# Optimization experiments

Hardware: AMD Instinct MI355X
Metric: run time of the kernel (lower is better)

## Reference

```python
import jax, jax.numpy as jnp
import numpy as np

NEG_SLOPE = 0.2

def setup_inputs() -> dict:
    key = jax.random.key(0)
    k1, k2, k3, k4, k5 = jax.random.split(key, 5)
    N_src, N_dst, E, H, D = 50000, 50000, 1600000, 8, 16
    return {
        "h_src": jax.random.normal(k1, (N_src, H * D), dtype=jnp.float32),
        "h_dst": jax.random.normal(k2, (N_dst, H * D), dtype=jnp.float32),
        "attn_l": jax.random.normal(k3, (1, H, D), dtype=jnp.float32),
        "src": jax.random.randint(k4, (E,), 0, N_src, dtype=jnp.int32),
        "dst": jax.random.randint(k5, (E,), 0, N_dst, dtype=jnp.int32),
    }

def reference(h_src, h_dst, attn_l, src, dst):
    N_dst = h_dst.shape[0]
    H, D = attn_l.shape[1], attn_l.shape[2]
    hs = h_src.reshape(-1, H, D)                       # [N_src, H, D]
    el = jnp.sum(hs * attn_l, axis=-1)                 # [N_src, H] per-node attn logit
    e = jax.nn.leaky_relu(el[src], NEG_SLOPE)          # [E, H] per-edge score
    # edge softmax over incoming edges of each dst node (stable)
    seg_max = jax.ops.segment_max(e, dst, num_segments=N_dst)   # [N_dst, H]
    ex = jnp.exp(e - seg_max[dst])                     # [E, H]
    denom = jax.ops.segment_sum(ex, dst, num_segments=N_dst)    # [N_dst, H]
    a = ex / denom[dst]                                # [E, H]
    # gather-multiply-scatter: u_mul_e then sum by dst
    m = hs[src] * a[:, :, None]                        # [E, H, D]
    out = jax.ops.segment_sum(m, dst, num_segments=N_dst)       # [N_dst, H, D]
    return out.reshape(N_dst, H * D)
```

## Files before the change

### kernel.cpp

```cpp
#include <hip/hip_runtime.h>

#define Hh 8
#define HD 128
#define NEG_SLOPE 0.2f
#define EPB 4096
#define GRS 197


__device__ __forceinline__ unsigned bfr(float f) {
    unsigned u = __float_as_uint(f);
    return (u + 0x7fffu + ((u >> 16) & 1u)) >> 16;
}
__device__ __forceinline__ unsigned pk(float a, float b) { return bfr(a) | (bfr(b) << 16); }

__global__ void __launch_bounds__(1024)
k1(const int* __restrict__ src, const int* __restrict__ dst,
   unsigned* __restrict__ tmp, unsigned short* __restrict__ ghs,
   int* __restrict__ bktTot, int E, int nblk,
   const float* __restrict__ hs, const float* __restrict__ attn,
   float* __restrict__ ew, uint4* __restrict__ hsb, int nh_src) {
    int t = threadIdx.x;
    if ((int)blockIdx.x < nblk) {
        __shared__ unsigned wbuf[EPB];
        __shared__ int lh[256], cur[256];
        int blk = blockIdx.x;
        int base = blk * EPB;
        int cnt = E - base; if (cnt > EPB) cnt = EPB;
        if (t < 256) lh[t] = 0;
        __syncthreads();
        int i = t * 4;
        bool vec = (i + 3 < cnt);
        if (vec) {
            int4 d = *(const int4*)(dst + base + i);
            int4 s = *(const int4*)(src + base + i);
            uint4 w;
            w.x = ((unsigned)d.x << 16) | (unsigned)s.x;
            w.y = ((unsigned)d.y << 16) | (unsigned)s.y;
            w.z = ((unsigned)d.z << 16) | (unsigned)s.z;
            w.w = ((unsigned)d.w << 16) | (unsigned)s.w;
            ((uint4*)wbuf)[t] = w;
            atomicAdd(&lh[d.x >> 8], 1);
            atomicAdd(&lh[d.y >> 8], 1);
            atomicAdd(&lh[d.z >> 8], 1);
            atomicAdd(&lh[d.w >> 8], 1);
        } else {
            for (int e = i; e < cnt; ++e) {
                int d = dst[base + e];
                wbuf[e] = ((unsigned)d << 16) | (unsigned)src[base + e];
                atomicAdd(&lh[d >> 8], 1);
            }
        }
        __syncthreads();
        int v = 0;
        if (t < 256) { v = lh[t]; cur[t] = v; }
        __syncthreads();
        for (int off = 1; off < 256; off <<= 1) {
            int x = 0;
            if (t < 256 && t >= off) x = cur[t - off];
            __syncthreads();
            if (t < 256) cur[t] += x;
            __syncthreads();
        }
        if (t < GRS) ghs[(size_t)blk * GRS + t] = (unsigned short)(cur[t] - ((t < 256) ? v : 0));
        if (t < 196 && v) atomicAdd(&bktTot[t], v);
        if (t < 256) cur[t] -= v;
        __syncthreads();
        if (vec) {
            uint4 w = ((uint4*)wbuf)[t];
            int p;
            p = atomicAdd(&cur[w.x >> 24], 1); tmp[base + p] = w.x;
            p = atomicAdd(&cur[w.y >> 24], 1); tmp[base + p] = w.y;
            p = atomicAdd(&cur[w.z >> 24], 1); tmp[base + p] = w.z;
            p = atomicAdd(&cur[w.w >> 24], 1); tmp[base + p] = w.w;
        } else {
            for (int e = i; e < cnt; ++e) {
                unsigned w = wbuf[e];
                int p = atomicAdd(&cur[w >> 24], 1);
                tmp[base + p] = w;
            }
        }
    } else {
        int i = ((int)blockIdx.x - nblk) * 1024 + t;
        if (i >= nh_src) return;
        int n = i >> 3, h = i & 7;
        const float4* a = (const float4*)(hs + (size_t)n * HD + h * 16);
        const float4* w = (const float4*)(attn + h * 16);
        float4 x0 = a[0], x1 = a[1], x2 = a[2], x3 = a[3];
        float4 w0 = w[0], w1 = w[1], w2 = w[2], w3 = w[3];
        float sv = x0.x * w0.x + x0.y * w0.y + x0.z * w0.z + x0.w * w0.w
                 + x1.x * w1.x + x1.y * w1.y + x1.z * w1.z + x1.w * w1.w
                 + x2.x * w2.x + x2.y * w2.y + x2.z * w2.z + x2.w * w2.w
                 + x3.x * w3.x + x3.y * w3.y + x3.z * w3.z + x3.w * w3.w;
        sv = (sv >= 0.f) ? sv : NEG_SLOPE * sv;
        ew[i] = __expf(sv);
        uint4 p0 = { pk(x0.x, x0.y), pk(x0.z, x0.w), pk(x1.x, x1.y), pk(x1.z, x1.w) };
        uint4 p1 = { pk(x2.x, x2.y), pk(x2.z, x2.w), pk(x3.x, x3.y), pk(x3.z, x3.w) };
        hsb[(size_t)n * 16 + h * 2]     = p0;
        hsb[(size_t)n * 16 + h * 2 + 1] = p1;
    }
}

__global__ void __launch_bounds__(1024)
k2(const unsigned* __restrict__ tmp, const unsigned short* __restrict__ ghs,
   const int* __restrict__ bktTot, unsigned short* __restrict__ adj,
   int* __restrict__ row_ptr, int E, int nblk, int nbkt, int ndst) {
    __shared__ int lh[256], sh[256], cur[256];
    __shared__ int base_s;
    int b = blockIdx.x, t = threadIdx.x;
    if (t < 256) lh[t] = 0;
    __syncthreads();
    for (int blk = t; blk < nblk; blk += 1024) {
        const unsigned short* gr = ghs + (size_t)blk * GRS;
        int st = gr[b], en = gr[b + 1];
        const unsigned* tp = tmp + (size_t)blk * EPB;
        for (int j = st; j < en; ++j)
            atomicAdd(&lh[(tp[j] >> 16) & 255], 1);
    }
    __syncthreads();
    int bc = 0;
    if (t < 256) { bc = (t < nbkt) ? bktTot[t] : 0; sh[t] = bc; }
    __syncthreads();
    for (int off = 1; off < 256; off <<= 1) {
        int x = 0;
        if (t < 256 && t >= off) x = sh[t - off];
        __syncthreads();
        if (t < 256) sh[t] += x;
        __syncthreads();
    }
    if (t == b) base_s = sh[t] - bc;
    __syncthreads();
    int base_b = base_s;
    int v = 0;
    if (t < 256) { v = lh[t]; sh[t] = v; }
    __syncthreads();
    for (int off = 1; off < 256; off <<= 1) {
        int x = 0;
        if (t < 256 && t >= off) x = sh[t - off];
        __syncthreads();
        if (t < 256) sh[t] += x;
        __syncthreads();
    }
    if (t < 256) {
        int start = base_b + sh[t] - v;
        cur[t] = start;
        int d = b * 256 + t;
        if (d < ndst) row_ptr[d] = start;
        if (b == 0 && t == 0) row_ptr[ndst] = E;
    }
    __syncthreads();
    for (int blk = t; blk < nblk; blk += 1024) {
        const unsigned short* gr = ghs + (size_t)blk * GRS;
        int st = gr[b], en = gr[b + 1];
        const unsigned* tp = tmp + (size_t)blk * EPB;
        for (int j = st; j < en; ++j) {
            unsigned w = tp[j];
            int pos = atomicAdd(&cur[(w >> 16) & 255], 1);
            adj[pos] = (unsigned short)(w & 0xffff);
        }
    }
}

#define ACC8(X, W) \
    a0.x += __uint_as_float((X).x << 16) * (W); \
    a0.y += __uint_as_float((X).x & 0xffff0000u) * (W); \
    a0.z += __uint_as_float((X).y << 16) * (W); \
    a0.w += __uint_as_float((X).y & 0xffff0000u) * (W); \
    a1.x += __uint_as_float((X).z << 16) * (W); \
    a1.y += __uint_as_float((X).z & 0xffff0000u) * (W); \
    a1.z += __uint_as_float((X).w << 16) * (W); \
    a1.w += __uint_as_float((X).w & 0xffff0000u) * (W);

__global__ void __launch_bounds__(128)
k_agg(const int* __restrict__ row_ptr, const unsigned short* __restrict__ adj,
      const uint4* __restrict__ hsb, const float* __restrict__ ew,
      float* __restrict__ out) {
    int d = blockIdx.x;
    int t = threadIdx.x;
    int j0 = row_ptr[d], j1 = row_ptr[d + 1];
    int q = t & 15;
    int slot = t >> 4;
    int h = q >> 1;

    float4 a0 = {0.f, 0.f, 0.f, 0.f}, a1 = {0.f, 0.f, 0.f, 0.f};
    float ws = 0.f;
    int j = j0 + slot;
    for (; j + 24 < j1; j += 32) {
        int s0 = adj[j], s1 = adj[j + 8], s2 = adj[j + 16], s3 = adj[j + 24];
        float w0 = ew[s0 * Hh + h], w1 = ew[s1 * Hh + h];
        float w2 = ew[s2 * Hh + h], w3 = ew[s3 * Hh + h];
        uint4 x0 = hsb[(size_t)s0 * 16 + q];
        uint4 x1 = hsb[(size_t)s1 * 16 + q];
        uint4 x2 = hsb[(size_t)s2 * 16 + q];
        uint4 x3 = hsb[(size_t)s3 * 16 + q];
        ACC8(x0, w0)
        ACC8(x1, w1)
        ACC8(x2, w2)
        ACC8(x3, w3)
        ws += w0 + w1 + w2 + w3;
    }
    for (; j < j1; j += 8) {
        int s0 = adj[j];
        float w0 = ew[s0 * Hh + h];
        uint4 x0 = hsb[(size_t)s0 * 16 + q];
        ACC8(x0, w0)
        ws += w0;
    }

#pragma unroll
    for (int off = 16; off <= 32; off <<= 1) {
        a0.x += __shfl_xor(a0.x, off, 64);
        a0.y += __shfl_xor(a0.y, off, 64);
        a0.z += __shfl_xor(a0.z, off, 64);
        a0.w += __shfl_xor(a0.w, off, 64);
        a1.x += __shfl_xor(a1.x, off, 64);
        a1.y += __shfl_xor(a1.y, off, 64);
        a1.z += __shfl_xor(a1.z, off, 64);
        a1.w += __shfl_xor(a1.w, off, 64);
        ws   += __shfl_xor(ws,   off, 64);
    }
    __shared__ float4 sp0[16], sp1[16];
    __shared__ float wsp[16];
    if (t >= 64 && t < 80) { sp0[q] = a0; sp1[q] = a1; wsp[q] = ws; }
    __syncthreads();
    if (t < 16) {
        float wt = ws + wsp[t];
        float r = (wt > 0.f) ? 1.0f / wt : 0.f;
        float4 o0 = sp0[t], o1 = sp1[t];
        o0.x = (a0.x + o0.x) * r; o0.y = (a0.y + o0.y) * r;
        o0.z = (a0.z + o0.z) * r; o0.w = (a0.w + o0.w) * r;
        o1.x = (a1.x + o1.x) * r; o1.y = (a1.y + o1.y) * r;
        o1.z = (a1.z + o1.z) * r; o1.w = (a1.w + o1.w) * r;
        float4* op = (float4*)(out + (size_t)d * HD + t * 8);
        op[0] = o0;
        op[1] = o1;
    }
}

extern "C" void kernel_launch(void* const* d_in, const int* in_sizes, int n_in,
                              void* d_out, int out_size, void* d_ws, size_t ws_size,
                              hipStream_t stream) {
    const float* h_src  = (const float*)d_in[0];
    const float* attn_l = (const float*)d_in[2];
    const int*   src    = (const int*)d_in[3];
    const int*   dst    = (const int*)d_in[4];
    float* out = (float*)d_out;

    const int N_src = in_sizes[0] / HD;
    const int N_dst = in_sizes[1] / HD;
    const int E     = in_sizes[3];
    const int NH_src = N_src * Hh;

    const int NBLK  = (E + EPB - 1) / EPB;
    const int NBKT  = (N_dst + 255) / 256;
    const int NB_EW = (NH_src + 1023) / 1024;

    unsigned short* hsb = (unsigned short*)d_ws;
    float* ew = (float*)(hsb + (size_t)N_src * HD);
    unsigned* tmp = (unsigned*)(ew + NH_src);
    unsigned short* adj = (unsigned short*)(tmp + (size_t)NBLK * EPB);
    unsigned short* ghs = adj + (((size_t)E + 1) & ~(size_t)1);
    int* bktTot  = (int*)(ghs + (((size_t)NBLK * GRS + 1) & ~(size_t)1));
    int* row_ptr = bktTot + 256;

    hipMemsetAsync(bktTot, 0, 256 * sizeof(int), stream);
    k1<<<NBLK + NB_EW, 1024, 0, stream>>>(src, dst, tmp, ghs, bktTot, E, NBLK,
                                          h_src, attn_l, ew, (uint4*)hsb, NH_src);
    k2<<<NBKT, 1024, 0, stream>>>(tmp, ghs, bktTot, adj, row_ptr,
                                  E, NBLK, NBKT, N_dst);
    k_agg<<<N_dst, 128, 0, stream>>>(row_ptr, adj, (const uint4*)hsb, ew, out);
}
```

Baseline: 213.1 us.

## Bin edges into fixed-capacity dst buckets and fuse local sort with aggregation

```diff
diff --git a/kernel.cpp b/kernel.cpp
--- a/kernel.cpp
+++ b/kernel.cpp
@@ -4,7 +4,7 @@
 #define HD 128
 #define NEG_SLOPE 0.2f
 #define EPB 4096
-#define GRS 197
+#define KCAP 2560
 
 
 __device__ __forceinline__ unsigned bfr(float f) {
@@ -15,18 +15,17 @@
 
 __global__ void __launch_bounds__(1024)
 k1(const int* __restrict__ src, const int* __restrict__ dst,
-   unsigned* __restrict__ tmp, unsigned short* __restrict__ ghs,
-   int* __restrict__ bktTot, int E, int nblk,
+   unsigned* __restrict__ tmp, int* __restrict__ blen,
+   int E, int nblk, int nbf,
    const float* __restrict__ hs, const float* __restrict__ attn,
    float* __restrict__ ew, uint4* __restrict__ hsb, int nh_src) {
     int t = threadIdx.x;
     if ((int)blockIdx.x < nblk) {
         __shared__ unsigned wbuf[EPB];
-        __shared__ int lh[256], cur[256];
-        int blk = blockIdx.x;
-        int base = blk * EPB;
+        __shared__ int lh[800], cur[800];
+        int base = blockIdx.x * EPB;
         int cnt = E - base; if (cnt > EPB) cnt = EPB;
-        if (t < 256) lh[t] = 0;
+        if (t < 800) lh[t] = 0;
         __syncthreads();
         int i = t * 4;
         bool vec = (i + 3 < cnt);
@@ -39,44 +38,36 @@
             w.z = ((unsigned)d.z << 16) | (unsigned)s.z;
             w.w = ((unsigned)d.w << 16) | (unsigned)s.w;
             ((uint4*)wbuf)[t] = w;
-            atomicAdd(&lh[d.x >> 8], 1);
-            atomicAdd(&lh[d.y >> 8], 1);
-            atomicAdd(&lh[d.z >> 8], 1);
-            atomicAdd(&lh[d.w >> 8], 1);
+            atomicAdd(&lh[d.x >> 6], 1);
+            atomicAdd(&lh[d.y >> 6], 1);
+            atomicAdd(&lh[d.z >> 6], 1);
+            atomicAdd(&lh[d.w >> 6], 1);
         } else {
             for (int e = i; e < cnt; ++e) {
                 int d = dst[base + e];
                 wbuf[e] = ((unsigned)d << 16) | (unsigned)src[base + e];
-                atomicAdd(&lh[d >> 8], 1);
+                atomicAdd(&lh[d >> 6], 1);
             }
         }
         __syncthreads();
-        int v = 0;
-        if (t < 256) { v = lh[t]; cur[t] = v; }
-        __syncthreads();
-        for (int off = 1; off < 256; off <<= 1) {
-            int x = 0;
-            if (t < 256 && t >= off) x = cur[t - off];
-            __syncthreads();
-            if (t < 256) cur[t] += x;
-            __syncthreads();
-        }
-        if (t < GRS) ghs[(size_t)blk * GRS + t] = (unsigned short)(cur[t] - ((t < 256) ? v : 0));
-        if (t < 196 && v) atomicAdd(&bktTot[t], v);
-        if (t < 256) cur[t] -= v;
+        if (t < nbf) cur[t] = atomicAdd(&blen[t * 16], lh[t]);
         __syncthreads();
         if (vec) {
             uint4 w = ((uint4*)wbuf)[t];
             int p;
-            p = atomicAdd(&cur[w.x >> 24], 1); tmp[base + p] = w.x;
-            p = atomicAdd(&cur[w.y >> 24], 1); tmp[base + p] = w.y;
-            p = atomicAdd(&cur[w.z >> 24], 1); tmp[base + p] = w.z;
-            p = atomicAdd(&cur[w.w >> 24], 1); tmp[base + p] = w.w;
+            p = atomicAdd(&cur[w.x >> 22], 1);
+            if (p < KCAP) tmp[(size_t)(w.x >> 22) * KCAP + p] = w.x;
+            p = atomicAdd(&cur[w.y >> 22], 1);
+            if (p < KCAP) tmp[(size_t)(w.y >> 22) * KCAP + p] = w.y;
+            p = atomicAdd(&cur[w.z >> 22], 1);
+            if (p < KCAP) tmp[(size_t)(w.z >> 22) * KCAP + p] = w.z;
+            p = atomicAdd(&cur[w.w >> 22], 1);
+            if (p < KCAP) tmp[(size_t)(w.w >> 22) * KCAP + p] = w.w;
         } else {
             for (int e = i; e < cnt; ++e) {
                 unsigned w = wbuf[e];
-                int p = atomicAdd(&cur[w >> 24], 1);
-                tmp[base + p] = w;
+                int p = atomicAdd(&cur[w >> 22], 1);
+                if (p < KCAP) tmp[(size_t)(w >> 22) * KCAP + p] = w;
             }
         }
     } else {
@@ -100,66 +91,6 @@
     }
 }
 
-__global__ void __launch_bounds__(1024)
-k2(const unsigned* __restrict__ tmp, const unsigned short* __restrict__ ghs,
-   const int* __restrict__ bktTot, unsigned short* __restrict__ adj,
-   int* __restrict__ row_ptr, int E, int nblk, int nbkt, int ndst) {
-    __shared__ int lh[256], sh[256], cur[256];
-    __shared__ int base_s;
-    int b = blockIdx.x, t = threadIdx.x;
-    if (t < 256) lh[t] = 0;
-    __syncthreads();
-    for (int blk = t; blk < nblk; blk += 1024) {
-        const unsigned short* gr = ghs + (size_t)blk * GRS;
-        int st = gr[b], en = gr[b + 1];
-        const unsigned* tp = tmp + (size_t)blk * EPB;
-        for (int j = st; j < en; ++j)
-            atomicAdd(&lh[(tp[j] >> 16) & 255], 1);
-    }
-    __syncthreads();
-    int bc = 0;
-    if (t < 256) { bc = (t < nbkt) ? bktTot[t] : 0; sh[t] = bc; }
-    __syncthreads();
-    for (int off = 1; off < 256; off <<= 1) {
-        int x = 0;
-        if (t < 256 && t >= off) x = sh[t - off];
-        __syncthreads();
-        if (t < 256) sh[t] += x;
-        __syncthreads();
-    }
-    if (t == b) base_s = sh[t] - bc;
-    __syncthreads();
-    int base_b = base_s;
-    int v = 0;
-    if (t < 256) { v = lh[t]; sh[t] = v; }
-    __syncthreads();
-    for (int off = 1; off < 256; off <<= 1) {
-        int x = 0;
-        if (t < 256 && t >= off) x = sh[t - off];
-        __syncthreads();
-        if (t < 256) sh[t] += x;
-        __syncthreads();
-    }
-    if (t < 256) {
-        int start = base_b + sh[t] - v;
-        cur[t] = start;
-        int d = b * 256 + t;
-        if (d < ndst) row_ptr[d] = start;
-        if (b == 0 && t == 0) row_ptr[ndst] = E;
-    }
-    __syncthreads();
-    for (int blk = t; blk < nblk; blk += 1024) {
-        const unsigned short* gr = ghs + (size_t)blk * GRS;
-        int st = gr[b], en = gr[b + 1];
-        const unsigned* tp = tmp + (size_t)blk * EPB;
-        for (int j = st; j < en; ++j) {
-            unsigned w = tp[j];
-            int pos = atomicAdd(&cur[(w >> 16) & 255], 1);
-            adj[pos] = (unsigned short)(w & 0xffff);
-        }
-    }
-}
-
 #define ACC8(X, W) \
     a0.x += __uint_as_float((X).x << 16) * (W); \
     a0.y += __uint_as_float((X).x & 0xffff0000u) * (W); \
@@ -170,69 +101,86 @@
     a1.z += __uint_as_float((X).w << 16) * (W); \
     a1.w += __uint_as_float((X).w & 0xffff0000u) * (W);
 
-__global__ void __launch_bounds__(128)
-k_agg(const int* __restrict__ row_ptr, const unsigned short* __restrict__ adj,
-      const uint4* __restrict__ hsb, const float* __restrict__ ew,
-      float* __restrict__ out) {
-    int d = blockIdx.x;
-    int t = threadIdx.x;
-    int j0 = row_ptr[d], j1 = row_ptr[d + 1];
-    int q = t & 15;
-    int slot = t >> 4;
-    int h = q >> 1;
-
-    float4 a0 = {0.f, 0.f, 0.f, 0.f}, a1 = {0.f, 0.f, 0.f, 0.f};
-    float ws = 0.f;
-    int j = j0 + slot;
-    for (; j + 24 < j1; j += 32) {
-        int s0 = adj[j], s1 = adj[j + 8], s2 = adj[j + 16], s3 = adj[j + 24];
-        float w0 = ew[s0 * Hh + h], w1 = ew[s1 * Hh + h];
-        float w2 = ew[s2 * Hh + h], w3 = ew[s3 * Hh + h];
-        uint4 x0 = hsb[(size_t)s0 * 16 + q];
-        uint4 x1 = hsb[(size_t)s1 * 16 + q];
-        uint4 x2 = hsb[(size_t)s2 * 16 + q];
-        uint4 x3 = hsb[(size_t)s3 * 16 + q];
-        ACC8(x0, w0)
-        ACC8(x1, w1)
-        ACC8(x2, w2)
-        ACC8(x3, w3)
-        ws += w0 + w1 + w2 + w3;
-    }
-    for (; j < j1; j += 8) {
-        int s0 = adj[j];
-        float w0 = ew[s0 * Hh + h];
-        uint4 x0 = hsb[(size_t)s0 * 16 + q];
-        ACC8(x0, w0)
-        ws += w0;
-    }
-
+__global__ void __launch_bounds__(1024)
+kA(const unsigned* __restrict__ tmp, const int* __restrict__ blen,
+   const uint4* __restrict__ hsb, const float* __restrict__ ew,
+   float* __restrict__ out, int ndst) {
+    __shared__ unsigned stg[KCAP], srt[KCAP];
+    __shared__ int lh[64], cur[64], exs[65];
+    int b = blockIdx.x, t = threadIdx.x;
+    int n = blen[b * 16]; if (n > KCAP) n = KCAP;
+    const unsigned* tp = tmp + (size_t)b * KCAP;
+    for (int j = t; j < n; j += 1024) stg[j] = tp[j];
+    if (t < 64) lh[t] = 0;
+    __syncthreads();
+    for (int j = t; j < n; j += 1024)
+        atomicAdd(&lh[(stg[j] >> 16) & 63], 1);
+    __syncthreads();
+    if (t == 0) {
+        int a = 0;
+        for (int k = 0; k < 64; ++k) { exs[k] = a; a += lh[k]; }
+        exs[64] = a;
+    }
+    __syncthreads();
+    if (t < 64) cur[t] = exs[t];
+    __syncthreads();
+    for (int j = t; j < n; j += 1024) {
+        unsigned w = stg[j];
+        int p = atomicAdd(&cur[(w >> 16) & 63], 1);
+        srt[p] = w;
+    }
+    __syncthreads();
+    int wave = t >> 6, lane = t & 63;
+    int q = lane & 15, slot = lane >> 4, h = q >> 1;
+    for (int ld = wave; ld < 64; ld += 16) {
+        int d = b * 64 + ld;
+        if (d >= ndst) break;
+        int j0 = exs[ld] + slot, j1 = exs[ld + 1];
+        float4 a0 = {0.f, 0.f, 0.f, 0.f}, a1 = {0.f, 0.f, 0.f, 0.f};
+        float ws = 0.f;
+        int j = j0;
+        for (; j + 12 < j1; j += 16) {
+            int s0 = srt[j] & 0xffff,      s1 = srt[j + 4] & 0xffff;
+            int s2 = srt[j + 8] & 0xffff,  s3 = srt[j + 12] & 0xffff;
+            float w0 = ew[s0 * Hh + h], w1 = ew[s1 * Hh + h];
+            float w2 = ew[s2 * Hh + h], w3 = ew[s3 * Hh + h];
+            uint4 x0 = hsb[(size_t)s0 * 16 + q];
+            uint4 x1 = hsb[(size_t)s1 * 16 + q];
+            uint4 x2 = hsb[(size_t)s2 * 16 + q];
+            uint4 x3 = hsb[(size_t)s3 * 16 + q];
+            ACC8(x0, w0)
+            ACC8(x1, w1)
+            ACC8(x2, w2)
+            ACC8(x3, w3)
+            ws += w0 + w1 + w2 + w3;
+        }
+        for (; j < j1; j += 4) {
+            int s0 = srt[j] & 0xffff;
+            float w0 = ew[s0 * Hh + h];
+            uint4 x0 = hsb[(size_t)s0 * 16 + q];
+            ACC8(x0, w0)
+            ws += w0;
+        }
 #pragma unroll
-    for (int off = 16; off <= 32; off <<= 1) {
-        a0.x += __shfl_xor(a0.x, off, 64);
-        a0.y += __shfl_xor(a0.y, off, 64);
-        a0.z += __shfl_xor(a0.z, off, 64);
-        a0.w += __shfl_xor(a0.w, off, 64);
-        a1.x += __shfl_xor(a1.x, off, 64);
-        a1.y += __shfl_xor(a1.y, off, 64);
-        a1.z += __shfl_xor(a1.z, off, 64);
-        a1.w += __shfl_xor(a1.w, off, 64);
-        ws   += __shfl_xor(ws,   off, 64);
-    }
-    __shared__ float4 sp0[16], sp1[16];
-    __shared__ float wsp[16];
-    if (t >= 64 && t < 80) { sp0[q] = a0; sp1[q] = a1; wsp[q] = ws; }
-    __syncthreads();
-    if (t < 16) {
-        float wt = ws + wsp[t];
-        float r = (wt > 0.f) ? 1.0f / wt : 0.f;
-        float4 o0 = sp0[t], o1 = sp1[t];
-        o0.x = (a0.x + o0.x) * r; o0.y = (a0.y + o0.y) * r;
-        o0.z = (a0.z + o0.z) * r; o0.w = (a0.w + o0.w) * r;
-        o1.x = (a1.x + o1.x) * r; o1.y = (a1.y + o1.y) * r;
-        o1.z = (a1.z + o1.z) * r; o1.w = (a1.w + o1.w) * r;
-        float4* op = (float4*)(out + (size_t)d * HD + t * 8);
-        op[0] = o0;
-        op[1] = o1;
+        for (int off = 16; off <= 32; off <<= 1) {
+            a0.x += __shfl_xor(a0.x, off, 64);
+            a0.y += __shfl_xor(a0.y, off, 64);
+            a0.z += __shfl_xor(a0.z, off, 64);
+            a0.w += __shfl_xor(a0.w, off, 64);
+            a1.x += __shfl_xor(a1.x, off, 64);
+            a1.y += __shfl_xor(a1.y, off, 64);
+            a1.z += __shfl_xor(a1.z, off, 64);
+            a1.w += __shfl_xor(a1.w, off, 64);
+            ws   += __shfl_xor(ws,   off, 64);
+        }
+        if (lane < 16) {
+            float r = (ws > 0.f) ? 1.0f / ws : 0.f;
+            a0.x *= r; a0.y *= r; a0.z *= r; a0.w *= r;
+            a1.x *= r; a1.y *= r; a1.z *= r; a1.w *= r;
+            float4* op = (float4*)(out + (size_t)d * HD + q * 8);
+            op[0] = a0;
+            op[1] = a1;
+        }
     }
 }
 
@@ -251,21 +199,16 @@
     const int NH_src = N_src * Hh;
 
     const int NBLK  = (E + EPB - 1) / EPB;
-    const int NBKT  = (N_dst + 255) / 256;
+    const int NBF   = (N_dst + 63) >> 6;
     const int NB_EW = (NH_src + 1023) / 1024;
 
     unsigned short* hsb = (unsigned short*)d_ws;
     float* ew = (float*)(hsb + (size_t)N_src * HD);
     unsigned* tmp = (unsigned*)(ew + NH_src);
-    unsigned short* adj = (unsigned short*)(tmp + (size_t)NBLK * EPB);
-    unsigned short* ghs = adj + (((size_t)E + 1) & ~(size_t)1);
-    int* bktTot  = (int*)(ghs + (((size_t)NBLK * GRS + 1) & ~(size_t)1));
-    int* row_ptr = bktTot + 256;
-
-    hipMemsetAsync(bktTot, 0, 256 * sizeof(int), stream);
-    k1<<<NBLK + NB_EW, 1024, 0, stream>>>(src, dst, tmp, ghs, bktTot, E, NBLK,
+    int* blen = (int*)(tmp + (size_t)NBF * KCAP);
+
+    hipMemsetAsync(blen, 0, (size_t)NBF * 16 * sizeof(int), stream);
+    k1<<<NBLK + NB_EW, 1024, 0, stream>>>(src, dst, tmp, blen, E, NBLK, NBF,
                                           h_src, attn_l, ew, (uint4*)hsb, NH_src);
-    k2<<<NBKT, 1024, 0, stream>>>(tmp, ghs, bktTot, adj, row_ptr,
-                                  E, NBLK, NBKT, N_dst);
-    k_agg<<<N_dst, 128, 0, stream>>>(row_ptr, adj, (const uint4*)hsb, ew, out);
-}
+    kA<<<NBF, 1024, 0, stream>>>(tmp, blen, (const uint4*)hsb, ew, out, N_dst);
+}
```

Result: faster. 194.9 us (-8.5%).
